# Kernel tuning notes

Measured on AMD Instinct MI355X. Metric: run time of the kernel, lower is better.

Reference implementation:

```python
import jax, jax.numpy as jnp
import numpy as np

N_NODES = 50000
N_EDGES = 1600000
CHANNELS = 128
EXPANSION = 50
CUTOFF = 5.0
LOG2 = 0.6931471805599453


def shifted_softplus(x):
    return jax.nn.softplus(x) - LOG2


def gaussian_smearing(r, cutoff=CUTOFF, n=EXPANSION):
    # centers evenly spaced in [0, cutoff]; width set by spacing
    centers = jnp.linspace(0.0, cutoff, n, dtype=r.dtype)
    delta = centers[1] - centers[0]
    coef = 1.0 / (2.0 * delta * delta)
    d = r[:, None] - centers[None, :]          # [E, n]
    return jnp.exp(-coef * d * d)


def setup_inputs() -> dict:
    key = jax.random.key(0)
    ks = jax.random.split(key, 12)
    C, F = CHANNELS, EXPANSION

    def lin(k, fan_in, shape):
        bound = 1.0 / np.sqrt(fan_in)
        return jax.random.uniform(k, shape, jnp.float32, -bound, bound)

    return {
        "features": jax.random.normal(ks[0], (N_NODES, C), jnp.float32),
        "edge_distances": jax.random.uniform(ks[1], (N_EDGES,), jnp.float32) * CUTOFF,
        "W_lin": lin(ks[2], C, (C, C)),
        "Wf1": lin(ks[3], F, (F, C)), "bf1": lin(ks[4], F, (C,)),
        "Wf2": lin(ks[5], C, (C, C)), "bf2": lin(ks[6], C, (C,)),
        "Wm1": lin(ks[7], C, (C, C)), "bm1": lin(ks[8], C, (C,)),
        "Wm2": lin(ks[9], C, (C, C)), "bm2": lin(ks[10], C, (C,)),
        "senders": jax.random.randint(ks[11], (N_EDGES,), 0, N_NODES, jnp.int32),
        "receivers": jax.random.randint(jax.random.fold_in(key, 99), (N_EDGES,), 0, N_NODES, jnp.int32),
    }


def reference(features, edge_distances, W_lin, Wf1, bf1, Wf2, bf2,
              Wm1, bm1, Wm2, bm2, senders, receivers):
    # 1. linear transform of node features (no bias)
    h = features @ W_lin.T                                   # [N, C]
    # 2. learnable radial filter F(r_ij): Gaussian basis -> MLP
    basis = gaussian_smearing(edge_distances)                # [E, F]
    ef = shifted_softplus(basis @ Wf1 + bf1) @ Wf2 + bf2     # [E, C]
    # 3. gather neighbour features, elementwise multiply, scatter-sum
    messages = h[senders] * ef                               # [E, C]
    agg = jax.ops.segment_sum(messages, receivers, num_segments=N_NODES)  # [N, C]
    # 4. output MLP
    return shifted_softplus(agg @ Wm1 + bm1) @ Wm2 + bm2
```

## Files before the change

kernel.cpp:

```cpp
#include <hip/hip_runtime.h>
#include <hip/hip_bf16.h>
#include <math.h>

#define N_NODES 50000
#define N_EDGES 1600000
#define CH 128
#define NF 50
#define NR 8192
#define NB 2048
#define BUCKET_NODES 25
#define CAP 1024
#define PASSA_CHUNK 4096
#define NBLK_SCAT 391
#define NBLK_TB   128
#define NBLK_DH   782

constexpr float DELTA  = 5.0f / 49.0f;
constexpr float COEF   = 1.0f / (2.0f * DELTA * DELTA);
constexpr float LOG2_  = 0.6931471805599453f;
constexpr float RSCALE = (float)(NR - 1) / 5.0f;

typedef short  bf16x8 __attribute__((ext_vector_type(8)));
typedef float  f32x4  __attribute__((ext_vector_type(4)));
typedef unsigned short ushort_t;
typedef unsigned long long u64;

__device__ __forceinline__ float ssp(float x) {
    return fmaxf(x, 0.0f) + __logf(1.0f + __expf(-fabsf(x))) - LOG2_;
}
__device__ __forceinline__ ushort_t f2bf(float x) {
    __hip_bfloat16 b = __float2bfloat16(x);
    return *reinterpret_cast<ushort_t*>(&b);
}
__device__ __forceinline__ float bf2f(ushort_t u) {
    return __uint_as_float(((unsigned)u) << 16);
}
__device__ __forceinline__ float4 f4zero() { return make_float4(0.f, 0.f, 0.f, 0.f); }

__global__ __launch_bounds__(256) void k1_prep(const float* __restrict__ Wlin,
                                               const float* __restrict__ Wm1,
                                               const float* __restrict__ Wm2,
                                               const float* __restrict__ Wf1,
                                               const float* __restrict__ Wf2,
                                               ushort_t* __restrict__ wlhi,
                                               ushort_t* __restrict__ wllo,
                                               ushort_t* __restrict__ wm1hi,
                                               ushort_t* __restrict__ wm1lo,
                                               ushort_t* __restrict__ wm2hi,
                                               ushort_t* __restrict__ wm2lo,
                                               ushort_t* __restrict__ wf1t,
                                               ushort_t* __restrict__ wf2hi,
                                               ushort_t* __restrict__ wf2lo,
                                               int* __restrict__ bcnt) {
    const int tid = threadIdx.x;
    if (blockIdx.x == 64) {
        for (int i = tid; i < NB; i += 256) bcnt[i] = 0;
        return;
    }
    int idx = blockIdx.x * 256 + tid;
    int n = idx >> 7, k = idx & 127;
    {   float w = Wlin[(size_t)n * CH + k];
        ushort_t hi = f2bf(w); wlhi[n * CH + k] = hi; wllo[n * CH + k] = f2bf(w - bf2f(hi)); }
    {   float w = Wm1[(size_t)k * CH + n];
        ushort_t hi = f2bf(w); wm1hi[n * CH + k] = hi; wm1lo[n * CH + k] = f2bf(w - bf2f(hi)); }
    {   float w = Wm2[(size_t)k * CH + n];
        ushort_t hi = f2bf(w); wm2hi[n * CH + k] = hi; wm2lo[n * CH + k] = f2bf(w - bf2f(hi)); }
    if (k < 64) wf1t[n * 64 + k] = (k < NF) ? f2bf(Wf1[k * CH + n]) : (ushort_t)0;
    {   float w = Wf2[(size_t)k * CH + n];
        ushort_t hi = f2bf(w); wf2hi[n * CH + k] = hi; wf2lo[n * CH + k] = f2bf(w - bf2f(hi)); }
}

__device__ void scatter_body(char* smem, int blk,
                             const int* __restrict__ recv,
                             const int* __restrict__ send,
                             const float* __restrict__ dist,
                             int* __restrict__ bcnt,
                             u64* __restrict__ brec) {
    int* bcur   = (int*)smem;
    int* bbaseL = bcur + NB;
    const int tid = threadIdx.x;
    for (int i = tid; i < NB; i += 256) bcur[i] = 0;
    __syncthreads();
    const int e0 = blk * PASSA_CHUNK;
#pragma unroll
    for (int i = 0; i < 16; i++) {
        int e = e0 + tid + i * 256;
        if (e < N_EDGES) atomicAdd(&bcur[recv[e] / BUCKET_NODES], 1);
    }
    __syncthreads();
    for (int i = tid; i < NB; i += 256) {
        int c = bcur[i];
        bbaseL[i] = c ? atomicAdd(&bcnt[i], c) : 0;
        bcur[i] = 0;
    }
    __syncthreads();
#pragma unroll
    for (int i = 0; i < 16; i++) {
        int e = e0 + tid + i * 256;
        if (e < N_EDGES) {
            int r = recv[e];
            int b = r / BUCKET_NODES;
            int rank = bbaseL[b] + atomicAdd(&bcur[b], 1);
            if (rank < CAP) {
                float x = fminf(dist[e] * RSCALE, (float)(NR - 1));
                int ti = __float2int_rn(x);
                u64 rec = (u64)(unsigned)(send[e] | (r << 16)) | ((u64)ti << 32);
                __builtin_nontemporal_store(rec, &brec[(size_t)b * CAP + rank]);
            }
        }
    }
}

__device__ void table_body(char* smem, int blk,
                           const float* __restrict__ bf1,
                           const float* __restrict__ bf2,
                           const ushort_t* __restrict__ wf1t,
                           const ushort_t* __restrict__ wf2hi,
                           const ushort_t* __restrict__ wf2lo,
                           ushort_t* __restrict__ tabn) {
    ushort_t (*basis)[72] = (ushort_t (*)[72])smem;
    ushort_t (*t1s)[136]  = (ushort_t (*)[136])(smem + 64 * 72 * 2);
    const int tid = threadIdx.x;
    const int g0  = blk * 64;

    for (int i = tid; i < 64 * 64; i += 256) {
        int e = i >> 6, k = i & 63;
        float val = 0.f;
        if (k < NF) {
            float r = (float)(g0 + e) * (5.0f / (float)(NR - 1));
            float d = r - (float)k * DELTA;
            val = __expf(-COEF * d * d);
        }
        basis[e][k] = f2bf(val);
    }
    __syncthreads();

    const int lane = tid & 63;
    const int wv   = tid >> 6;
    const int row  = lane & 15;
    const int quad = lane >> 4;
    const int c0   = (2 * wv) * 16 + row;
    const int c1   = c0 + 16;

    f32x4 acc[2][4];
#pragma unroll
    for (int j = 0; j < 2; j++)
#pragma unroll
        for (int rt = 0; rt < 4; rt++) acc[j][rt] = (f32x4){0.f, 0.f, 0.f, 0.f};

#pragma unroll
    for (int kb = 0; kb < 64; kb += 32) {
        bf16x8 B0 = *(const bf16x8*)&wf1t[c0 * 64 + kb + quad * 8];
        bf16x8 B1 = *(const bf16x8*)&wf1t[c1 * 64 + kb + quad * 8];
#pragma unroll
        for (int rt = 0; rt < 4; rt++) {
            bf16x8 A = *(const bf16x8*)&basis[rt * 16 + row][kb + quad * 8];
            acc[0][rt] = __builtin_amdgcn_mfma_f32_16x16x32_bf16(A, B0, acc[0][rt], 0, 0, 0);
            acc[1][rt] = __builtin_amdgcn_mfma_f32_16x16x32_bf16(A, B1, acc[1][rt], 0, 0, 0);
        }
    }
    {
        float b1v[2] = { bf1[c0], bf1[c1] };
#pragma unroll
        for (int j = 0; j < 2; j++) {
            int c = j ? c1 : c0;
#pragma unroll
            for (int rt = 0; rt < 4; rt++)
#pragma unroll
                for (int rg = 0; rg < 4; rg++) {
                    int e = rt * 16 + quad * 4 + rg;
                    t1s[e][c] = f2bf(ssp(acc[j][rt][rg] + b1v[j]));
                }
        }
    }
    __syncthreads();

#pragma unroll
    for (int j = 0; j < 2; j++)
#pragma unroll
        for (int rt = 0; rt < 4; rt++) acc[j][rt] = (f32x4){0.f, 0.f, 0.f, 0.f};

#pragma unroll
    for (int kb = 0; kb < 128; kb += 32) {
        bf16x8 B0h = *(const bf16x8*)&wf2hi[c0 * CH + kb + quad * 8];
        bf16x8 B0l = *(const bf16x8*)&wf2lo[c0 * CH + kb + quad * 8];
        bf16x8 B1h = *(const bf16x8*)&wf2hi[c1 * CH + kb + quad * 8];
        bf16x8 B1l = *(const bf16x8*)&wf2lo[c1 * CH + kb + quad * 8];
#pragma unroll
        for (int rt = 0; rt < 4; rt++) {
            bf16x8 A = *(const bf16x8*)&t1s[rt * 16 + row][kb + quad * 8];
            acc[0][rt] = __builtin_amdgcn_mfma_f32_16x16x32_bf16(A, B0l, acc[0][rt], 0, 0, 0);
            acc[0][rt] = __builtin_amdgcn_mfma_f32_16x16x32_bf16(A, B0h, acc[0][rt], 0, 0, 0);
            acc[1][rt] = __builtin_amdgcn_mfma_f32_16x16x32_bf16(A, B1l, acc[1][rt], 0, 0, 0);
            acc[1][rt] = __builtin_amdgcn_mfma_f32_16x16x32_bf16(A, B1h, acc[1][rt], 0, 0, 0);
        }
    }
    {
        float b2v[2] = { bf2[c0], bf2[c1] };
#pragma unroll
        for (int j = 0; j < 2; j++) {
            int c = j ? c1 : c0;
#pragma unroll
            for (int rt = 0; rt < 4; rt++)
#pragma unroll
                for (int rg = 0; rg < 4; rg++) {
                    int g = g0 + rt * 16 + quad * 4 + rg;
                    tabn[(size_t)g * CH + c] = f2bf(acc[j][rt][rg] + b2v[j]);
                }
        }
    }
}

__device__ void dense_h_body(char* smem, int blk,
                             const float* __restrict__ X,
                             const ushort_t* __restrict__ Bhi,
                             const ushort_t* __restrict__ Blo,
                             ushort_t* __restrict__ Y) {
    ushort_t (*xs)[136] = (ushort_t (*)[136])smem;
    const int tid  = threadIdx.x;
    const int row0 = blk * 64;

#pragma unroll
    for (int i = 0; i < 8; i++) {
        int idx = tid + i * 256;
        int r   = idx >> 5;
        int c4  = (idx & 31) * 4;
        float4 v = (row0 + r < N_NODES) ? *(const float4*)&X[(size_t)(row0 + r) * CH + c4]
                                        : f4zero();
        ushort4 s;
        s.x = f2bf(v.x); s.y = f2bf(v.y); s.z = f2bf(v.z); s.w = f2bf(v.w);
        *(ushort4*)&xs[r][c4] = s;
    }
    __syncthreads();

    const int lane = tid & 63;
    const int wv   = tid >> 6;
    const int row  = lane & 15;
    const int quad = lane >> 4;
    const int c0   = (2 * wv) * 16 + row;
    const int c1   = c0 + 16;

    f32x4 acc[2][4];
#pragma unroll
    for (int j = 0; j < 2; j++)
#pragma unroll
        for (int rt = 0; rt < 4; rt++) acc[j][rt] = (f32x4){0.f, 0.f, 0.f, 0.f};

#pragma unroll
    for (int kb = 0; kb < 128; kb += 32) {
        bf16x8 B0h = *(const bf16x8*)&Bhi[(size_t)c0 * CH + kb + quad * 8];
        bf16x8 B0l = *(const bf16x8*)&Blo[(size_t)c0 * CH + kb + quad * 8];
        bf16x8 B1h = *(const bf16x8*)&Bhi[(size_t)c1 * CH + kb + quad * 8];
        bf16x8 B1l = *(const bf16x8*)&Blo[(size_t)c1 * CH + kb + quad * 8];
#pragma unroll
        for (int rt = 0; rt < 4; rt++) {
            bf16x8 A = *(const bf16x8*)&xs[rt * 16 + row][kb + quad * 8];
            acc[0][rt] = __builtin_amdgcn_mfma_f32_16x16x32_bf16(A, B0l, acc[0][rt], 0, 0, 0);
            acc[0][rt] = __builtin_amdgcn_mfma_f32_16x16x32_bf16(A, B0h, acc[0][rt], 0, 0, 0);
            acc[1][rt] = __builtin_amdgcn_mfma_f32_16x16x32_bf16(A, B1l, acc[1][rt], 0, 0, 0);
            acc[1][rt] = __builtin_amdgcn_mfma_f32_16x16x32_bf16(A, B1h, acc[1][rt], 0, 0, 0);
        }
    }

#pragma unroll
    for (int j = 0; j < 2; j++) {
        int c = j ? c1 : c0;
#pragma unroll
        for (int rt = 0; rt < 4; rt++)
#pragma unroll
            for (int rg = 0; rg < 4; rg++) {
                int r = row0 + rt * 16 + quad * 4 + rg;
                if (r < N_NODES) Y[(size_t)r * CH + c] = f2bf(acc[j][rt][rg]);
            }
    }
}

__global__ __launch_bounds__(256) void k2_mega(const int* __restrict__ recv,
                                               const int* __restrict__ send,
                                               const float* __restrict__ dist,
                                               int* __restrict__ bcnt,
                                               u64* __restrict__ brec,
                                               const float* __restrict__ bf1,
                                               const float* __restrict__ bf2,
                                               const ushort_t* __restrict__ wf1t,
                                               const ushort_t* __restrict__ wf2hi,
                                               const ushort_t* __restrict__ wf2lo,
                                               ushort_t* __restrict__ tabn,
                                               const float* __restrict__ X,
                                               const ushort_t* __restrict__ wlhi,
                                               const ushort_t* __restrict__ wllo,
                                               ushort_t* __restrict__ h) {
    __shared__ __align__(16) char smem[64 * 72 * 2 + 64 * 136 * 2];
    const int blk = blockIdx.x;
    if (blk < NBLK_SCAT) {
        scatter_body(smem, blk, recv, send, dist, bcnt, brec);
    } else if (blk < NBLK_SCAT + NBLK_TB) {
        table_body(smem, blk - NBLK_SCAT, bf1, bf2, wf1t, wf2hi, wf2lo, tabn);
    } else {
        dense_h_body(smem, blk - NBLK_SCAT - NBLK_TB, X, wlhi, wllo, h);
    }
}

__global__ __launch_bounds__(256) void sort_gather_mlp(const int* __restrict__ bcnt,
                                                       const u64* __restrict__ brec,
                                                       const ushort_t* __restrict__ h,
                                                       const ushort_t* __restrict__ tabn,
                                                       const ushort_t* __restrict__ B1hi,
                                                       const ushort_t* __restrict__ B1lo,
                                                       const float* __restrict__ bm1,
                                                       const ushort_t* __restrict__ B2hi,
                                                       const ushort_t* __restrict__ B2lo,
                                                       const float* __restrict__ bm2,
                                                       float* __restrict__ OUT) {
    __shared__ int shist[BUCKET_NODES];
    __shared__ int sbeg[BUCKET_NODES];
    __shared__ int sexc[BUCKET_NODES];
    __shared__ unsigned sout[CAP];
    __shared__ __align__(16) ushort_t at[32][136];
    const int b = blockIdx.x, tid = threadIdx.x;
    const int nbase = b * BUCKET_NODES;
    const int nn = min(BUCKET_NODES, N_NODES - nbase);
    if (nn <= 0) return;
    const int m = min(bcnt[b], CAP);
    const u64* my = brec + (size_t)b * CAP;

    for (int i = tid; i < nn; i += 256) shist[i] = 0;
    for (int i = tid; i < 32 * 17; i += 256) {
        bf16x8 z = (bf16x8){0, 0, 0, 0, 0, 0, 0, 0};
        *(bf16x8*)&at[i / 17][(i % 17) * 8] = z;
    }
    __syncthreads();
    for (int i = tid; i < m; i += 256) {
        u64 rec = __builtin_nontemporal_load(&my[i]);
        int l = (int)((rec >> 16) & 0xFFFF) - nbase;
        atomicAdd(&shist[l], 1);
    }
    __syncthreads();
    if (tid == 0) {
        int acc = 0;
#pragma unroll
        for (int l = 0; l < BUCKET_NODES; l++) {
            if (l < nn) { sexc[l] = acc; sbeg[l] = acc; acc += shist[l]; }
        }
    }
    __syncthreads();
    for (int i = tid; i < m; i += 256) {
        u64 rec = __builtin_nontemporal_load(&my[i]);
        int l = (int)((rec >> 16) & 0xFFFF) - nbase;
        int rank = atomicAdd(&sexc[l], 1);
        sout[rank] = (unsigned)(rec & 0xFFFF) | ((unsigned)((rec >> 32) & 0x3FFF) << 16);
    }
    __syncthreads();

    {
        const int g  = tid >> 4;
        const int c8 = (tid & 15) * 8;
        for (int l = g; l < nn; l += 16) {
            const int beg = sbeg[l], end = sbeg[l] + shist[l];
            float acc[8];
#pragma unroll
            for (int j = 0; j < 8; j++) acc[j] = 0.f;

            int e = beg;
            for (; e + 8 <= end; e += 8) {
                unsigned v[8];
#pragma unroll
                for (int u = 0; u < 8; u++) v[u] = sout[e + u];
                bf16x8 hu[8], tn[8];
#pragma unroll
                for (int u = 0; u < 8; u++) {
                    int s  = (int)(v[u] & 0xFFFF);
                    int ti = (int)(v[u] >> 16);
                    hu[u] = *(const bf16x8*)&h[(size_t)s * CH + c8];
                    tn[u] = *(const bf16x8*)&tabn[(size_t)ti * CH + c8];
                }
#pragma unroll
                for (int u = 0; u < 8; u++)
#pragma unroll
                    for (int j = 0; j < 8; j++)
                        acc[j] = fmaf(bf2f((ushort_t)hu[u][j]), bf2f((ushort_t)tn[u][j]), acc[j]);
            }
            for (; e + 4 <= end; e += 4) {
                unsigned v[4];
#pragma unroll
                for (int u = 0; u < 4; u++) v[u] = sout[e + u];
                bf16x8 hu[4], tn[4];
#pragma unroll
                for (int u = 0; u < 4; u++) {
                    int s  = (int)(v[u] & 0xFFFF);
                    int ti = (int)(v[u] >> 16);
                    hu[u] = *(const bf16x8*)&h[(size_t)s * CH + c8];
                    tn[u] = *(const bf16x8*)&tabn[(size_t)ti * CH + c8];
                }
#pragma unroll
                for (int u = 0; u < 4; u++)
#pragma unroll
                    for (int j = 0; j < 8; j++)
                        acc[j] = fmaf(bf2f((ushort_t)hu[u][j]), bf2f((ushort_t)tn[u][j]), acc[j]);
            }
            for (; e < end; e++) {
                unsigned v = sout[e];
                int s  = (int)(v & 0xFFFF);
                int ti = (int)(v >> 16);
                bf16x8 hu = *(const bf16x8*)&h[(size_t)s * CH + c8];
                bf16x8 tn = *(const bf16x8*)&tabn[(size_t)ti * CH + c8];
#pragma unroll
                for (int j = 0; j < 8; j++)
                    acc[j] = fmaf(bf2f((ushort_t)hu[j]), bf2f((ushort_t)tn[j]), acc[j]);
            }

            bf16x8 o;
#pragma unroll
            for (int j = 0; j < 8; j++) o[j] = (short)f2bf(acc[j]);
            *(bf16x8*)&at[l][c8] = o;
        }
    }
    __syncthreads();

    const int lane = tid & 63;
    const int wv   = tid >> 6;
    const int row  = lane & 15;
    const int quad = lane >> 4;
    const int c0   = (2 * wv) * 16 + row;
    const int c1   = c0 + 16;

    f32x4 acc[2][2];
#pragma unroll
    for (int j = 0; j < 2; j++)
#pragma unroll
        for (int rt = 0; rt < 2; rt++) acc[j][rt] = (f32x4){0.f, 0.f, 0.f, 0.f};

#pragma unroll
    for (int kb = 0; kb < 128; kb += 32) {
        bf16x8 B0h = *(const bf16x8*)&B1hi[(size_t)c0 * CH + kb + quad * 8];
        bf16x8 B0l = *(const bf16x8*)&B1lo[(size_t)c0 * CH + kb + quad * 8];
        bf16x8 B1h_ = *(const bf16x8*)&B1hi[(size_t)c1 * CH + kb + quad * 8];
        bf16x8 B1l_ = *(const bf16x8*)&B1lo[(size_t)c1 * CH + kb + quad * 8];
#pragma unroll
        for (int rt = 0; rt < 2; rt++) {
            bf16x8 A = *(const bf16x8*)&at[rt * 16 + row][kb + quad * 8];
            acc[0][rt] = __builtin_amdgcn_mfma_f32_16x16x32_bf16(A, B0l, acc[0][rt], 0, 0, 0);
            acc[0][rt] = __builtin_amdgcn_mfma_f32_16x16x32_bf16(A, B0h, acc[0][rt], 0, 0, 0);
            acc[1][rt] = __builtin_amdgcn_mfma_f32_16x16x32_bf16(A, B1l_, acc[1][rt], 0, 0, 0);
            acc[1][rt] = __builtin_amdgcn_mfma_f32_16x16x32_bf16(A, B1h_, acc[1][rt], 0, 0, 0);
        }
    }
    __syncthreads();
    {
        float bv[2] = { bm1[c0], bm1[c1] };
#pragma unroll
        for (int j = 0; j < 2; j++) {
            int c = j ? c1 : c0;
#pragma unroll
            for (int rt = 0; rt < 2; rt++)
#pragma unroll
                for (int rg = 0; rg < 4; rg++)
                    at[rt * 16 + quad * 4 + rg][c] = f2bf(ssp(acc[j][rt][rg] + bv[j]));
        }
    }
    __syncthreads();

#pragma unroll
    for (int j = 0; j < 2; j++)
#pragma unroll
        for (int rt = 0; rt < 2; rt++) acc[j][rt] = (f32x4){0.f, 0.f, 0.f, 0.f};

#pragma unroll
    for (int kb = 0; kb < 128; kb += 32) {
        bf16x8 B0h = *(const bf16x8*)&B2hi[(size_t)c0 * CH + kb + quad * 8];
        bf16x8 B0l = *(const bf16x8*)&B2lo[(size_t)c0 * CH + kb + quad * 8];
        bf16x8 B1h_ = *(const bf16x8*)&B2hi[(size_t)c1 * CH + kb + quad * 8];
        bf16x8 B1l_ = *(const bf16x8*)&B2lo[(size_t)c1 * CH + kb + quad * 8];
#pragma unroll
        for (int rt = 0; rt < 2; rt++) {
            bf16x8 A = *(const bf16x8*)&at[rt * 16 + row][kb + quad * 8];
            acc[0][rt] = __builtin_amdgcn_mfma_f32_16x16x32_bf16(A, B0l, acc[0][rt], 0, 0, 0);
            acc[0][rt] = __builtin_amdgcn_mfma_f32_16x16x32_bf16(A, B0h, acc[0][rt], 0, 0, 0);
            acc[1][rt] = __builtin_amdgcn_mfma_f32_16x16x32_bf16(A, B1l_, acc[1][rt], 0, 0, 0);
            acc[1][rt] = __builtin_amdgcn_mfma_f32_16x16x32_bf16(A, B1h_, acc[1][rt], 0, 0, 0);
        }
    }
    {
        float bv[2] = { bm2[c0], bm2[c1] };
#pragma unroll
        for (int j = 0; j < 2; j++) {
            int c = j ? c1 : c0;
#pragma unroll
            for (int rt = 0; rt < 2; rt++)
#pragma unroll
                for (int rg = 0; rg < 4; rg++) {
                    int r = rt * 16 + quad * 4 + rg;
                    if (r < nn) OUT[(size_t)(nbase + r) * CH + c] = acc[j][rt][rg] + bv[j];
                }
        }
    }
}

extern "C" void kernel_launch(void* const* d_in, const int* in_sizes, int n_in,
                              void* d_out, int out_size, void* d_ws, size_t ws_size,
                              hipStream_t stream) {
    const float* features = (const float*)d_in[0];
    const float* dist     = (const float*)d_in[1];
    const float* W_lin    = (const float*)d_in[2];
    const float* Wf1      = (const float*)d_in[3];
    const float* bf1      = (const float*)d_in[4];
    const float* Wf2      = (const float*)d_in[5];
    const float* bf2      = (const float*)d_in[6];
    const float* Wm1      = (const float*)d_in[7];
    const float* bm1      = (const float*)d_in[8];
    const float* Wm2      = (const float*)d_in[9];
    const float* bm2      = (const float*)d_in[10];
    const int* senders    = (const int*)d_in[11];
    const int* receivers  = (const int*)d_in[12];
    float* out = (float*)d_out;

    u64* brec       = (u64*)d_ws;
    ushort_t* h     = (ushort_t*)(brec + (size_t)NB * CAP);
    ushort_t* tabn  = h + (size_t)N_NODES * CH;
    int* bcnt       = (int*)(tabn + (size_t)NR * CH);
    ushort_t* wlhi  = (ushort_t*)(bcnt + NB);
    ushort_t* wllo  = wlhi  + CH * CH;
    ushort_t* wm1hi = wllo  + CH * CH;
    ushort_t* wm1lo = wm1hi + CH * CH;
    ushort_t* wm2hi = wm1lo + CH * CH;
    ushort_t* wm2lo = wm2hi + CH * CH;
    ushort_t* wf1t  = wm2lo + CH * CH;
    ushort_t* wf2hi = wf1t  + CH * 64;
    ushort_t* wf2lo = wf2hi + CH * CH;

    k1_prep<<<65, 256, 0, stream>>>(W_lin, Wm1, Wm2, Wf1, Wf2,
                                    wlhi, wllo, wm1hi, wm1lo, wm2hi, wm2lo,
                                    wf1t, wf2hi, wf2lo, bcnt);

    k2_mega<<<NBLK_SCAT + NBLK_TB + NBLK_DH, 256, 0, stream>>>(
        receivers, senders, dist, bcnt, brec,
        bf1, bf2, wf1t, wf2hi, wf2lo, tabn,
        features, wlhi, wllo, h);

    sort_gather_mlp<<<NB, 256, 0, stream>>>(bcnt, brec, h, tabn,
                                            wm1hi, wm1lo, bm1,
                                            wm2hi, wm2lo, bm2, out);
}
```

Baseline: 270.1 us.

## Balance edge gather across groups with flat edge ranges and shared float atomics

The bucket size goes from 25 to 32 nodes (NB 1563, CAP 1280) so the 32-row MFMA tile is fully used. Each 16-thread group now takes an equal slice of the bucket's sorted edges instead of whole nodes, flushing partial sums into a float shared-memory accumulator with atomics at node boundaries. This removes load imbalance from uneven node degrees. Bucket records are loaded once into registers and reused for both the histogram and the scatter, and the nontemporal hints are dropped. The cost is extra LDS atomics, a float-to-bf16 conversion on the A-operand loads, and more shared memory.

Result: faster. 264.3 us (-2.2%).

```diff
diff --git a/kernel.cpp b/kernel.cpp
--- a/kernel.cpp
+++ b/kernel.cpp
@@ -7,9 +7,9 @@
 #define CH 128
 #define NF 50
 #define NR 8192
-#define NB 2048
-#define BUCKET_NODES 25
-#define CAP 1024
+#define NB 1563
+#define BUCKET_NODES 32
+#define CAP 1280
 #define PASSA_CHUNK 4096
 #define NBLK_SCAT 391
 #define NBLK_TB   128
@@ -105,7 +105,7 @@
                 float x = fminf(dist[e] * RSCALE, (float)(NR - 1));
                 int ti = __float2int_rn(x);
                 u64 rec = (u64)(unsigned)(send[e] | (r << 16)) | ((u64)ti << 32);
-                __builtin_nontemporal_store(rec, &brec[(size_t)b * CAP + rank]);
+                brec[(size_t)b * CAP + rank] = rec;
             }
         }
     }
@@ -316,7 +316,7 @@
     __shared__ int sbeg[BUCKET_NODES];
     __shared__ int sexc[BUCKET_NODES];
     __shared__ unsigned sout[CAP];
-    __shared__ __align__(16) ushort_t at[32][136];
+    __shared__ __align__(16) float atf[32][132];
     const int b = blockIdx.x, tid = threadIdx.x;
     const int nbase = b * BUCKET_NODES;
     const int nn = min(BUCKET_NODES, N_NODES - nbase);
@@ -324,95 +324,100 @@
     const int m = min(bcnt[b], CAP);
     const u64* my = brec + (size_t)b * CAP;
 
-    for (int i = tid; i < nn; i += 256) shist[i] = 0;
-    for (int i = tid; i < 32 * 17; i += 256) {
-        bf16x8 z = (bf16x8){0, 0, 0, 0, 0, 0, 0, 0};
-        *(bf16x8*)&at[i / 17][(i % 17) * 8] = z;
-    }
-    __syncthreads();
-    for (int i = tid; i < m; i += 256) {
-        u64 rec = __builtin_nontemporal_load(&my[i]);
-        int l = (int)((rec >> 16) & 0xFFFF) - nbase;
-        atomicAdd(&shist[l], 1);
+    if (tid < BUCKET_NODES) shist[tid] = 0;
+    for (int i = tid; i < 1056; i += 256) ((float4*)atf)[i] = f4zero();
+    __syncthreads();
+
+    unsigned pw0 = 0, pw1 = 0, pw2 = 0, pw3 = 0, pw4 = 0;
+    int lc0 = -1, lc1 = -1, lc2 = -1, lc3 = -1, lc4 = -1;
+    {
+        int i;
+        i = tid;           if (i < m) { u64 rec = my[i]; lc0 = (int)((rec >> 16) & 0xFFFF) - nbase; pw0 = (unsigned)(rec & 0xFFFF) | ((unsigned)((rec >> 32) & 0x3FFF) << 16); }
+        i = tid + 256;     if (i < m) { u64 rec = my[i]; lc1 = (int)((rec >> 16) & 0xFFFF) - nbase; pw1 = (unsigned)(rec & 0xFFFF) | ((unsigned)((rec >> 32) & 0x3FFF) << 16); }
+        i = tid + 512;     if (i < m) { u64 rec = my[i]; lc2 = (int)((rec >> 16) & 0xFFFF) - nbase; pw2 = (unsigned)(rec & 0xFFFF) | ((unsigned)((rec >> 32) & 0x3FFF) << 16); }
+        i = tid + 768;     if (i < m) { u64 rec = my[i]; lc3 = (int)((rec >> 16) & 0xFFFF) - nbase; pw3 = (unsigned)(rec & 0xFFFF) | ((unsigned)((rec >> 32) & 0x3FFF) << 16); }
+        i = tid + 1024;    if (i < m) { u64 rec = my[i]; lc4 = (int)((rec >> 16) & 0xFFFF) - nbase; pw4 = (unsigned)(rec & 0xFFFF) | ((unsigned)((rec >> 32) & 0x3FFF) << 16); }
+        if (lc0 >= 0) atomicAdd(&shist[lc0], 1);
+        if (lc1 >= 0) atomicAdd(&shist[lc1], 1);
+        if (lc2 >= 0) atomicAdd(&shist[lc2], 1);
+        if (lc3 >= 0) atomicAdd(&shist[lc3], 1);
+        if (lc4 >= 0) atomicAdd(&shist[lc4], 1);
     }
     __syncthreads();
     if (tid == 0) {
         int acc = 0;
 #pragma unroll
         for (int l = 0; l < BUCKET_NODES; l++) {
-            if (l < nn) { sexc[l] = acc; sbeg[l] = acc; acc += shist[l]; }
-        }
-    }
-    __syncthreads();
-    for (int i = tid; i < m; i += 256) {
-        u64 rec = __builtin_nontemporal_load(&my[i]);
-        int l = (int)((rec >> 16) & 0xFFFF) - nbase;
-        int rank = atomicAdd(&sexc[l], 1);
-        sout[rank] = (unsigned)(rec & 0xFFFF) | ((unsigned)((rec >> 32) & 0x3FFF) << 16);
-    }
-    __syncthreads();
-
-    {
-        const int g  = tid >> 4;
-        const int c8 = (tid & 15) * 8;
-        for (int l = g; l < nn; l += 16) {
-            const int beg = sbeg[l], end = sbeg[l] + shist[l];
-            float acc[8];
-#pragma unroll
-            for (int j = 0; j < 8; j++) acc[j] = 0.f;
-
-            int e = beg;
-            for (; e + 8 <= end; e += 8) {
-                unsigned v[8];
-#pragma unroll
-                for (int u = 0; u < 8; u++) v[u] = sout[e + u];
-                bf16x8 hu[8], tn[8];
-#pragma unroll
-                for (int u = 0; u < 8; u++) {
-                    int s  = (int)(v[u] & 0xFFFF);
-                    int ti = (int)(v[u] >> 16);
-                    hu[u] = *(const bf16x8*)&h[(size_t)s * CH + c8];
-                    tn[u] = *(const bf16x8*)&tabn[(size_t)ti * CH + c8];
+            sexc[l] = acc; sbeg[l] = acc; acc += shist[l];
+        }
+    }
+    __syncthreads();
+    {
+        if (lc0 >= 0) { int rank = atomicAdd(&sexc[lc0], 1); sout[rank] = pw0; }
+        if (lc1 >= 0) { int rank = atomicAdd(&sexc[lc1], 1); sout[rank] = pw1; }
+        if (lc2 >= 0) { int rank = atomicAdd(&sexc[lc2], 1); sout[rank] = pw2; }
+        if (lc3 >= 0) { int rank = atomicAdd(&sexc[lc3], 1); sout[rank] = pw3; }
+        if (lc4 >= 0) { int rank = atomicAdd(&sexc[lc4], 1); sout[rank] = pw4; }
+    }
+    __syncthreads();
+
+    {
+        const int g   = tid >> 4;
+        const int c8  = (tid & 15) * 8;
+        const int per = (m + 15) >> 4;
+        const int e0g = g * per;
+        const int e1g = min(m, e0g + per);
+
+        float acc[8];
+#pragma unroll
+        for (int j = 0; j < 8; j++) acc[j] = 0.f;
+        int l = 0;
+        while (l < nn && sbeg[l] + shist[l] <= e0g) l++;
+
+        int e = e0g;
+        for (; e + 8 <= e1g; e += 8) {
+            unsigned v[8];
+#pragma unroll
+            for (int u = 0; u < 8; u++) v[u] = sout[e + u];
+            bf16x8 hu[8], tn[8];
+#pragma unroll
+            for (int u = 0; u < 8; u++) {
+                int s  = (int)(v[u] & 0xFFFF);
+                int ti = (int)(v[u] >> 16);
+                hu[u] = *(const bf16x8*)&h[(size_t)s * CH + c8];
+                tn[u] = *(const bf16x8*)&tabn[(size_t)ti * CH + c8];
+            }
+#pragma unroll
+            for (int u = 0; u < 8; u++) {
+                int ee = e + u;
+                while (ee >= sbeg[l] + shist[l]) {
+#pragma unroll
+                    for (int j = 0; j < 8; j++) { atomicAdd(&atf[l][c8 + j], acc[j]); acc[j] = 0.f; }
+                    l++;
                 }
 #pragma unroll
-                for (int u = 0; u < 8; u++)
-#pragma unroll
-                    for (int j = 0; j < 8; j++)
-                        acc[j] = fmaf(bf2f((ushort_t)hu[u][j]), bf2f((ushort_t)tn[u][j]), acc[j]);
+                for (int j = 0; j < 8; j++)
+                    acc[j] = fmaf(bf2f((ushort_t)hu[u][j]), bf2f((ushort_t)tn[u][j]), acc[j]);
             }
-            for (; e + 4 <= end; e += 4) {
-                unsigned v[4];
-#pragma unroll
-                for (int u = 0; u < 4; u++) v[u] = sout[e + u];
-                bf16x8 hu[4], tn[4];
-#pragma unroll
-                for (int u = 0; u < 4; u++) {
-                    int s  = (int)(v[u] & 0xFFFF);
-                    int ti = (int)(v[u] >> 16);
-                    hu[u] = *(const bf16x8*)&h[(size_t)s * CH + c8];
-                    tn[u] = *(const bf16x8*)&tabn[(size_t)ti * CH + c8];
-                }
-#pragma unroll
-                for (int u = 0; u < 4; u++)
-#pragma unroll
-                    for (int j = 0; j < 8; j++)
-                        acc[j] = fmaf(bf2f((ushort_t)hu[u][j]), bf2f((ushort_t)tn[u][j]), acc[j]);
+        }
+        for (; e < e1g; e++) {
+            unsigned v = sout[e];
+            while (e >= sbeg[l] + shist[l]) {
+#pragma unroll
+                for (int j = 0; j < 8; j++) { atomicAdd(&atf[l][c8 + j], acc[j]); acc[j] = 0.f; }
+                l++;
             }
-            for (; e < end; e++) {
-                unsigned v = sout[e];
-                int s  = (int)(v & 0xFFFF);
-                int ti = (int)(v >> 16);
-                bf16x8 hu = *(const bf16x8*)&h[(size_t)s * CH + c8];
-                bf16x8 tn = *(const bf16x8*)&tabn[(size_t)ti * CH + c8];
-#pragma unroll
-                for (int j = 0; j < 8; j++)
-                    acc[j] = fmaf(bf2f((ushort_t)hu[j]), bf2f((ushort_t)tn[j]), acc[j]);
-            }
-
-            bf16x8 o;
-#pragma unroll
-            for (int j = 0; j < 8; j++) o[j] = (short)f2bf(acc[j]);
-            *(bf16x8*)&at[l][c8] = o;
+            int s  = (int)(v & 0xFFFF);
+            int ti = (int)(v >> 16);
+            bf16x8 hu = *(const bf16x8*)&h[(size_t)s * CH + c8];
+            bf16x8 tn = *(const bf16x8*)&tabn[(size_t)ti * CH + c8];
+#pragma unroll
+            for (int j = 0; j < 8; j++)
+                acc[j] = fmaf(bf2f((ushort_t)hu[j]), bf2f((ushort_t)tn[j]), acc[j]);
+        }
+        if (e1g > e0g && l < nn) {
+#pragma unroll
+            for (int j = 0; j < 8; j++) atomicAdd(&atf[l][c8 + j], acc[j]);
         }
     }
     __syncthreads();
@@ -438,7 +443,10 @@
         bf16x8 B1l_ = *(const bf16x8*)&B1lo[(size_t)c1 * CH + kb + quad * 8];
 #pragma unroll
         for (int rt = 0; rt < 2; rt++) {
-            bf16x8 A = *(const bf16x8*)&at[rt * 16 + row][kb + quad * 8];
+            const float* ap = &atf[rt * 16 + row][kb + quad * 8];
+            bf16x8 A;
+#pragma unroll
+            for (int j = 0; j < 8; j++) A[j] = (short)f2bf(ap[j]);
             acc[0][rt] = __builtin_amdgcn_mfma_f32_16x16x32_bf16(A, B0l, acc[0][rt], 0, 0, 0);
             acc[0][rt] = __builtin_amdgcn_mfma_f32_16x16x32_bf16(A, B0h, acc[0][rt], 0, 0, 0);
             acc[1][rt] = __builtin_amdgcn_mfma_f32_16x16x32_bf16(A, B1l_, acc[1][rt], 0, 0, 0);
@@ -446,6 +454,7 @@
         }
     }
     __syncthreads();
+    ushort_t (*ts)[136] = (ushort_t (*)[136])atf;
     {
         float bv[2] = { bm1[c0], bm1[c1] };
 #pragma unroll
@@ -455,7 +464,7 @@
             for (int rt = 0; rt < 2; rt++)
 #pragma unroll
                 for (int rg = 0; rg < 4; rg++)
-                    at[rt * 16 + quad * 4 + rg][c] = f2bf(ssp(acc[j][rt][rg] + bv[j]));
+                    ts[rt * 16 + quad * 4 + rg][c] = f2bf(ssp(acc[j][rt][rg] + bv[j]));
         }
     }
     __syncthreads();
@@ -473,7 +482,7 @@
         bf16x8 B1l_ = *(const bf16x8*)&B2lo[(size_t)c1 * CH + kb + quad * 8];
 #pragma unroll
         for (int rt = 0; rt < 2; rt++) {
-            bf16x8 A = *(const bf16x8*)&at[rt * 16 + row][kb + quad * 8];
+            bf16x8 A = *(const bf16x8*)&ts[rt * 16 + row][kb + quad * 8];
             acc[0][rt] = __builtin_amdgcn_mfma_f32_16x16x32_bf16(A, B0l, acc[0][rt], 0, 0, 0);
             acc[0][rt] = __builtin_amdgcn_mfma_f32_16x16x32_bf16(A, B0h, acc[0][rt], 0, 0, 0);
             acc[1][rt] = __builtin_amdgcn_mfma_f32_16x16x32_bf16(A, B1l_, acc[1][rt], 0, 0, 0);
```
